# Performance work log

Measured on AMD Instinct MI355X. Metric: run time of the kernel, lower is better.

The kernel has to match this reference:

```python
import jax, jax.numpy as jnp
import numpy as np

B, D = 4096, 1024
N_CLASSES = 100
INF = jnp.float32(3.4e38)


def setup_inputs() -> dict:
    key = jax.random.key(0)
    k1, k2 = jax.random.split(key)
    x = jax.random.normal(k1, (B, 1, D), dtype=jnp.float32)
    labels = jax.random.randint(k2, (B,), 0, N_CLASSES)
    return {"x": x, "labels": labels}


def _awareness_scan(xs, labels_f, R_init):
    # xs: [B, D] float32, labels_f: [B] float32
    b, d = xs.shape
    slots = jnp.arange(b)

    def step(state, inp):
        refs, ref_labels, n_refs, count, min_d, max_d, R = state
        xi, li = inp
        mask = slots < n_refs  # active reference slots
        # distances from candidate to current reference set (torch.cdist, p=2)
        d_all = jnp.sqrt(jnp.sum((refs - xi[None, :]) ** 2, axis=-1))  # [B]
        d_all = jax.lax.stop_gradient(d_all)
        d_act = jnp.where(mask, d_all, INF)
        min_act = jnp.min(d_act)
        is_first = count == 1
        # new reference iff ALL active distances exceed R (i.e. min > R)
        insert = is_first | (min_act > R)
        refs2 = jnp.where(insert, refs.at[n_refs].set(xi), refs)
        ref_labels2 = jnp.where(insert, ref_labels.at[n_refs].set(li), ref_labels)
        n_refs2 = n_refs + insert.astype(n_refs.dtype)
        # dynamic ray update (skipped on the very first sample, as in torch)
        max_act = jnp.max(jnp.where(mask, d_all, -INF))
        min_d2 = jnp.where(is_first, min_d, jnp.minimum(min_d, min_act))
        max_d2 = jnp.where(is_first, max_d, jnp.maximum(max_d, max_act))
        R2 = jnp.where(is_first, R, (min_d2 + max_d2) / 3)
        # prediction: nearest reference AFTER potential insertion
        mask2 = slots < n_refs2
        d2 = jnp.sqrt(jnp.sum((refs2 - xi[None, :]) ** 2, axis=-1))
        d2 = jax.lax.stop_gradient(d2)
        idx = jnp.argmin(jnp.where(mask2, d2, INF))
        pred = ref_labels2[idx]
        new_state = (refs2, ref_labels2, n_refs2, count + 1, min_d2, max_d2, R2)
        return new_state, pred

    init = (
        jnp.zeros((b, d), jnp.float32),   # reference instances buffer
        jnp.zeros((b,), jnp.float32),     # reference labels buffer
        jnp.int32(0),                     # n_refs
        jnp.int32(1),                     # count (starts at 1, as in torch)
        INF,                              # min_dist
        jnp.float32(0.0),                 # max_dist
        jnp.float32(R_init),              # R
    )
    _, preds = jax.lax.scan(step, init, (xs, labels_f))
    return preds  # [B] float32


def reference(x, labels):
    # x: [B, 1, D]; labels: [B] int. update_ref_insts=True, set_labels=labels.
    xs = x.reshape(x.shape[0], x.shape[2])
    labels_f = labels.astype(jnp.float32)
    return _awareness_scan(xs, labels_f, 1.0)
```

## Files before the change

### kernel.cpp

```cpp
#include <hip/hip_runtime.h>
#include <stdint.h>

#define B_N   4096
#define D_DIM 1024
#define INF_F 3.4e38f
#define NT    64
#define NBLK  (NT * (NT + 1) / 2)

typedef float floatx4 __attribute__((ext_vector_type(4)));

#define XQ_OFF 131072

__global__ __launch_bounds__(256)
void k_prep(const float* __restrict__ x, unsigned char* __restrict__ xq,
            float* __restrict__ norms,
            unsigned long long* __restrict__ minpack,
            unsigned int* __restrict__ maxbits) {
    const int row = blockIdx.x;
    const int t   = threadIdx.x;
    float4 v = ((const float4*)x)[row * 256 + t];
    int p = __builtin_amdgcn_cvt_pk_fp8_f32(v.x, v.y, 0, false);
    p     = __builtin_amdgcn_cvt_pk_fp8_f32(v.z, v.w, p, true);
    ((int*)xq)[row * 256 + t] = p;
    float s = v.x * v.x + v.y * v.y + v.z * v.z + v.w * v.w;
    #pragma unroll
    for (int off = 32; off; off >>= 1) s += __shfl_down(s, off);
    __shared__ float ws4[4];
    if ((t & 63) == 0) ws4[t >> 6] = s;
    __syncthreads();
    if (t == 0) {
        norms[row]   = ws4[0] + ws4[1] + ws4[2] + ws4[3];
        minpack[row] = 0xFFFFFFFFFFFFFFFFull;
        maxbits[row] = 0u;
    }
}

#define GLDS(g, l)                                                              \
    __builtin_amdgcn_global_load_lds(                                           \
        (__attribute__((address_space(1))) void*)(void*)(g),                    \
        (__attribute__((address_space(3))) void*)(void*)(l), 16, 0, 0)

__global__ __launch_bounds__(128, 3)
void k_pass1(const unsigned char* __restrict__ xq,
             const float* __restrict__ norms,
             unsigned long long* __restrict__ minpack,
             unsigned int* __restrict__ maxbits) {
    int bid = blockIdx.x;
    int ti  = (int)((sqrtf(8.f * bid + 1.f) - 1.f) * 0.5f);
    while ((ti + 1) * (ti + 2) / 2 <= bid) ti++;
    while (ti * (ti + 1) / 2 > bid) ti--;
    int tj  = bid - ti * (ti + 1) / 2;

    __shared__ __align__(16) unsigned char lds[16384];

    const int t    = threadIdx.x;
    const int w    = t >> 6, lane = t & 63;
    const int q4   = lane >> 4, c15 = lane & 15;
    const int i0   = ti * 64, j0 = tj * 64;

    unsigned char* myA = lds + w * 8192;
    unsigned char* myB = myA + 4096;

    const int sr = lane >> 2;
    const int sc = (lane & 3) ^ (sr & 3);

    const unsigned char* gA[4]; const unsigned char* gB[4];
    #pragma unroll
    for (int e = 0; e < 4; e++) {
        int row = e * 16 + sr;
        size_t ko = (size_t)w * 512 + (size_t)sc * 16;
        gA[e] = xq + (size_t)(i0 + row) * D_DIM + ko;
        gB[e] = xq + (size_t)(j0 + row) * D_DIM + ko;
    }

    int foff[4][2];
    #pragma unroll
    for (int st = 0; st < 4; st++)
        #pragma unroll
        for (int kk = 0; kk < 2; kk++)
            foff[st][kk] = (st * 16 + c15) * 64 +
                           ((((kk << 1) | (q4 >> 1)) ^ (c15 & 3)) << 4) +
                           ((q4 & 1) << 3);

    floatx4 acc[4][4];
    #pragma unroll
    for (int m = 0; m < 4; m++)
        #pragma unroll
        for (int n = 0; n < 4; n++)
            acc[m][n] = (floatx4){0.f, 0.f, 0.f, 0.f};

    for (int it = 0; it < 8; it++) {
        #pragma unroll
        for (int e = 0; e < 4; e++) {
            GLDS(gA[e], myA + e * 1024);
            GLDS(gB[e], myB + e * 1024);
            gA[e] += 64; gB[e] += 64;
        }
        asm volatile("s_waitcnt vmcnt(0)" ::: "memory");
        #pragma unroll
        for (int kk = 0; kk < 2; kk++) {
            long long af[4], bfr[4];
            #pragma unroll
            for (int st = 0; st < 4; st++) {
                af[st]  = *(const long long*)(myA + foff[st][kk]);
                bfr[st] = *(const long long*)(myB + foff[st][kk]);
            }
            #pragma unroll
            for (int m = 0; m < 4; m++)
                #pragma unroll
                for (int n = 0; n < 4; n++)
                    acc[m][n] = __builtin_amdgcn_mfma_f32_16x16x32_fp8_fp8(
                        af[m], bfr[n], acc[m][n], 0, 0, 0);
        }
    }

    __syncthreads();
    float* cbuf = (float*)lds;
    if (w == 1) {
        #pragma unroll
        for (int m = 0; m < 4; m++)
            #pragma unroll
            for (int n = 0; n < 4; n++)
                #pragma unroll
                for (int r = 0; r < 4; r++)
                    cbuf[((m * 4 + n) * 4 + r) * 64 + lane] = acc[m][n][r];
    }
    __syncthreads();
    if (w == 0) {
        #pragma unroll
        for (int m = 0; m < 4; m++)
            #pragma unroll
            for (int n = 0; n < 4; n++)
                #pragma unroll
                for (int r = 0; r < 4; r++)
                    acc[m][n][r] += cbuf[((m * 4 + n) * 4 + r) * 64 + lane];

        float njv[4];
        #pragma unroll
        for (int n = 0; n < 4; n++) njv[n] = norms[j0 + n * 16 + c15];
        #pragma unroll
        for (int m = 0; m < 4; m++) {
            #pragma unroll
            for (int r = 0; r < 4; r++) {
                int gi   = i0 + m * 16 + q4 * 4 + r;
                float ni = norms[gi];
                unsigned long long mp = 0xFFFFFFFFFFFFFFFFull;
                float mx = -INF_F;
                #pragma unroll
                for (int n = 0; n < 4; n++) {
                    int gj = j0 + n * 16 + c15;
                    if (gj < gi) {
                        float d = sqrtf(fmaxf(ni + njv[n] - 2.f * acc[m][n][r], 0.f));
                        unsigned long long p =
                            ((unsigned long long)__float_as_uint(d) << 32) | (unsigned)gj;
                        if (p < mp) mp = p;
                        mx = fmaxf(mx, d);
                    }
                }
                #pragma unroll
                for (int off = 1; off < 16; off <<= 1) {
                    unsigned long long op = __shfl_xor(mp, off, 64);
                    if (op < mp) mp = op;
                    float om = __shfl_xor(mx, off, 64);
                    mx = fmaxf(mx, om);
                }
                if (c15 == 0 && mp != 0xFFFFFFFFFFFFFFFFull) {
                    atomicMin(&minpack[gi], mp);
                    atomicMax(&maxbits[gi], __float_as_uint(mx));
                }
            }
        }
    }
}

__global__ __launch_bounds__(1024)
void k_tail(const unsigned long long* __restrict__ minpack,
            const unsigned int* __restrict__ maxbits,
            const float* __restrict__ x, const float* __restrict__ norms,
            const int* __restrict__ labels, int* __restrict__ ref_idx,
            float* __restrict__ out) {
    const int t = threadIdx.x;
    float m[4], M[4];
    #pragma unroll
    for (int q = 0; q < 4; q++) {
        int i = t * 4 + q;
        unsigned long long p = minpack[i];
        float dmin = (p == 0xFFFFFFFFFFFFFFFFull)
                       ? INF_F : __uint_as_float((unsigned)(p >> 32));
        m[q] = (i == 0) ? INF_F : dmin;
        M[q] = (i == 0) ? -INF_F : __uint_as_float(maxbits[i]);
    }
    float pmin[4], pmax[4];
    pmin[0] = m[0]; pmax[0] = M[0];
    #pragma unroll
    for (int q = 1; q < 4; q++) {
        pmin[q] = fminf(pmin[q - 1], m[q]);
        pmax[q] = fmaxf(pmax[q - 1], M[q]);
    }
    __shared__ float smin[1024], smax[1024];
    smin[t] = pmin[3]; smax[t] = pmax[3];
    __syncthreads();
    for (int off = 1; off < 1024; off <<= 1) {
        float a = (t >= off) ? smin[t - off] : INF_F;
        float b = (t >= off) ? smax[t - off] : -INF_F;
        __syncthreads();
        smin[t] = fminf(smin[t], a);
        smax[t] = fmaxf(smax[t], b);
        __syncthreads();
    }
    float exMin = (t > 0) ? smin[t - 1] : INF_F;
    float exMax = (t > 0) ? smax[t - 1] : -INF_F;

    int viol = B_N;
    #pragma unroll
    for (int q = 0; q < 4; q++) {
        int i = t * 4 + q;
        if (i >= 1) {
            float pm = (q == 0) ? exMin : fminf(exMin, pmin[q - 1]);
            float pM = (q == 0) ? exMax : fmaxf(exMax, pmax[q - 1]);
            float R  = (i == 1) ? 1.0f : (pm + pM) / 3.0f;
            if (!(m[q] > R) && i < viol) viol = i;
        }
    }
    __shared__ int sv[1024];
    sv[t] = viol;
    __syncthreads();
    for (int off = 512; off; off >>= 1) {
        if (t < off) sv[t] = min(sv[t], sv[t + off]);
        __syncthreads();
    }
    const int s_star = sv[0];

    for (int i = t; i < s_star; i += 1024) out[i] = (float)labels[i];

    __shared__ float s_state[3];
    __shared__ int s_n;
    if (s_star < B_N && t == (s_star >> 2)) {
        int q = s_star & 3;
        float pm = (q == 0) ? exMin : fminf(exMin, pmin[q - 1]);
        float pM = (q == 0) ? exMax : fmaxf(exMax, pmax[q - 1]);
        float md = fminf(pm, m[q]);
        float Md = fmaxf(pM, M[q]);
        s_state[0] = md; s_state[1] = Md; s_state[2] = (md + Md) / 3.0f;
        s_n = s_star;
        unsigned long long p = minpack[s_star];
        int j = (int)(unsigned)(p & 0xFFFFFFFFu);
        out[s_star] = (float)labels[j];
    }
    if (s_star >= B_N) return;

    for (int s = t; s < s_star; s += 1024) ref_idx[s] = s;
    __syncthreads();

    __shared__ unsigned long long redp[1024];
    __shared__ float redm[1024];
    for (int i = s_star + 1; i < B_N; i++) {
        int n = s_n;
        const float* xi = x + (size_t)i * D_DIM;
        float ni = norms[i];
        unsigned long long mp = 0xFFFFFFFFFFFFFFFFull;
        float mx = -INF_F;
        for (int slot = t; slot < n; slot += 1024) {
            int j = ref_idx[slot];
            const float* xj = x + (size_t)j * D_DIM;
            float dot = 0.f;
            for (int k = 0; k < D_DIM; k++) dot = fmaf(xi[k], xj[k], dot);
            float d = sqrtf(fmaxf(ni + norms[j] - 2.f * dot, 0.f));
            unsigned long long p =
                ((unsigned long long)__float_as_uint(d) << 32) | (unsigned)slot;
            if (p < mp) mp = p;
            mx = fmaxf(mx, d);
        }
        redp[t] = mp; redm[t] = mx;
        __syncthreads();
        for (int off = 512; off; off >>= 1) {
            if (t < off) {
                if (redp[t + off] < redp[t]) redp[t] = redp[t + off];
                redm[t] = fmaxf(redm[t], redm[t + off]);
            }
            __syncthreads();
        }
        if (t == 0) {
            unsigned long long p = redp[0];
            float min_act = __uint_as_float((unsigned)(p >> 32));
            int minslot   = (int)(unsigned)(p & 0xFFFFFFFFu);
            float max_act = redm[0];
            bool insert = (min_act > s_state[2]);
            int pred;
            if (insert) {
                ref_idx[n] = i;
                s_n = n + 1;
                pred = (min_act <= 0.0f) ? labels[ref_idx[minslot]] : labels[i];
            } else {
                pred = labels[ref_idx[minslot]];
            }
            float md = fminf(s_state[0], min_act);
            float Md = fmaxf(s_state[1], max_act);
            s_state[0] = md; s_state[1] = Md; s_state[2] = (md + Md) / 3.0f;
            out[i] = (float)pred;
        }
        __syncthreads();
    }
}

extern "C" void kernel_launch(void* const* d_in, const int* in_sizes, int n_in,
                              void* d_out, int out_size, void* d_ws, size_t ws_size,
                              hipStream_t stream) {
    const float* x      = (const float*)d_in[0];
    const int*   labels = (const int*)d_in[1];
    float*       out    = (float*)d_out;
    char* ws = (char*)d_ws;
    unsigned long long* minpack = (unsigned long long*)ws;
    unsigned int*       maxbits = (unsigned int*)(ws + 32768);
    float*              norms   = (float*)(ws + 49152);
    int*                ref_idx = (int*)(ws + 65600);
    unsigned char*      xq      = (unsigned char*)(ws + XQ_OFF);

    k_prep<<<B_N, 256, 0, stream>>>(x, xq, norms, minpack, maxbits);
    k_pass1<<<NBLK, 128, 0, stream>>>(xq, norms, minpack, maxbits);
    k_tail<<<1, 1024, 0, stream>>>(minpack, maxbits, x, norms, labels, ref_idx, out);
}
```

Measured before the change: 111.6 us.

## Triple-buffer LDS loads in pass1 to overlap global fetch with MFMA

Replaces the single-buffered load/wait/compute loop in k_pass1 with a three-slot LDS ring. Loads for two iterations ahead are issued, and graded vmcnt waits allow computation on the current slot while later loads are still in flight. Each block now uses three times the LDS, and launch bounds drop from 3 to 1 blocks per SM, which may reduce occupancy and the latency hiding it provided.

```diff
diff --git a/kernel.cpp b/kernel.cpp
--- a/kernel.cpp
+++ b/kernel.cpp
@@ -40,7 +40,7 @@
         (__attribute__((address_space(1))) void*)(void*)(g),                    \
         (__attribute__((address_space(3))) void*)(void*)(l), 16, 0, 0)
 
-__global__ __launch_bounds__(128, 3)
+__global__ __launch_bounds__(128, 1)
 void k_pass1(const unsigned char* __restrict__ xq,
              const float* __restrict__ norms,
              unsigned long long* __restrict__ minpack,
@@ -51,15 +51,19 @@
     while (ti * (ti + 1) / 2 > bid) ti--;
     int tj  = bid - ti * (ti + 1) / 2;
 
-    __shared__ __align__(16) unsigned char lds[16384];
+    __shared__ __align__(16) unsigned char lds[49152];
 
     const int t    = threadIdx.x;
     const int w    = t >> 6, lane = t & 63;
     const int q4   = lane >> 4, c15 = lane & 15;
     const int i0   = ti * 64, j0 = tj * 64;
 
-    unsigned char* myA = lds + w * 8192;
-    unsigned char* myB = myA + 4096;
+    unsigned char* bufA[3]; unsigned char* bufB[3];
+    #pragma unroll
+    for (int b = 0; b < 3; b++) {
+        bufA[b] = lds + w * 24576 + b * 8192;
+        bufB[b] = bufA[b] + 4096;
+    }
 
     const int sr = lane >> 2;
     const int sc = (lane & 3) ^ (sr & 3);
@@ -73,6 +77,17 @@
         gB[e] = xq + (size_t)(j0 + row) * D_DIM + ko;
     }
 
+#define ISSUE_BATCH(bslot, itk)                                                 \
+    do {                                                                        \
+        unsigned char* A_ = bufA[(bslot)];                                      \
+        unsigned char* B_ = bufB[(bslot)];                                      \
+        _Pragma("unroll")                                                       \
+        for (int e = 0; e < 4; e++) {                                           \
+            GLDS(gA[e] + (itk) * 64, A_ + e * 1024);                            \
+            GLDS(gB[e] + (itk) * 64, B_ + e * 1024);                            \
+        }                                                                       \
+    } while (0)
+
     int foff[4][2];
     #pragma unroll
     for (int st = 0; st < 4; st++)
@@ -89,14 +104,17 @@
         for (int n = 0; n < 4; n++)
             acc[m][n] = (floatx4){0.f, 0.f, 0.f, 0.f};
 
+    ISSUE_BATCH(0, 0);
+    ISSUE_BATCH(1, 1);
+
+    #pragma unroll
     for (int it = 0; it < 8; it++) {
-        #pragma unroll
-        for (int e = 0; e < 4; e++) {
-            GLDS(gA[e], myA + e * 1024);
-            GLDS(gB[e], myB + e * 1024);
-            gA[e] += 64; gB[e] += 64;
-        }
-        asm volatile("s_waitcnt vmcnt(0)" ::: "memory");
+        if (it + 2 < 8) ISSUE_BATCH((it + 2) % 3, it + 2);
+        if (it < 6)      asm volatile("s_waitcnt vmcnt(16)" ::: "memory");
+        else if (it == 6) asm volatile("s_waitcnt vmcnt(8)" ::: "memory");
+        else              asm volatile("s_waitcnt vmcnt(0)" ::: "memory");
+        const unsigned char* myA = bufA[it % 3];
+        const unsigned char* myB = bufB[it % 3];
         #pragma unroll
         for (int kk = 0; kk < 2; kk++) {
             long long af[4], bfr[4];
```

Result: slower. 137.6 us (+23.3%).
